# Optimization experiments

Measured on AMD Instinct MI355X. Metric: run time of the kernel, lower is better.

## Reference

```python
import jax, jax.numpy as jnp
import numpy as np


def setup_inputs() -> dict:
    key = jax.random.key(0)
    k1, k2 = jax.random.split(key)
    B, N, C, Hq, Wq = 4, 10, 256, 32, 32
    Hs, Ws = 32, 32
    return {
        "query_features": jax.random.normal(k1, (B, C, Hq, Wq), dtype=jnp.float32),
        "support_features": jax.random.normal(k2, (N, C, Hs, Ws), dtype=jnp.float32),
        "K": 5,
    }


def reference(query_features, support_features, K):
    B, C, Hq, Wq = query_features.shape
    N, _, Hs, Ws = support_features.shape
    Lq, Ls = Hq * Wq, Hs * Ws

    # [B, Lq, C] -> repeat over N -> [B*N, Lq, C]
    q = query_features.reshape(B, C, Lq).transpose(0, 2, 1)
    q = jnp.broadcast_to(q[:, None], (B, N, Lq, C)).reshape(B * N, Lq, C)
    # [N, C, Ls] -> repeat over B -> [B*N, C, Ls]
    s = support_features.reshape(N, C, Ls)
    s = jnp.broadcast_to(s[None], (B, N, C, Ls)).reshape(B * N, C, Ls)

    # global mean-centering (scalar mean over the whole repeated tensor)
    q = q - q.mean()
    s = s - s.mean()

    # unscaled similarity attention: QK^T -> softmax -> PV
    sim = jnp.einsum("bqc,bcs->bqs", q, s)          # [B*N, Lq, Ls]
    sim = jax.nn.softmax(sim, axis=-1)
    aligned = jnp.einsum("bqs,bcs->bqc", sim, s)    # [B*N, Lq, C]

    # average over K shots per class
    aligned = aligned.reshape(B, N // K, K, Hq, Wq, C).mean(axis=2)
    aligned = aligned.transpose(1, 0, 4, 2, 3)      # [N//K, B, C, Hq, Wq]

    q_out = q.transpose(0, 2, 1).reshape(B, N // K, K, C, Hq, Wq).mean(axis=2)
    # q_out: [B, N//K, C, Hq, Wq]
    return q_out, aligned
```

## Files before the change

kernel.cpp:

```cpp
#include <hip/hip_runtime.h>

#define CQ_ELEMS (4 * 256 * 1024)
#define CS_ELEMS (10 * 256 * 1024)
#define OUT2_OFF 2097152

typedef __attribute__((ext_vector_type(8))) _Float16 f16x8;
typedef __attribute__((ext_vector_type(4))) float f32x4;

#define WS_SH 256
#define SH_ELEMS (10 * 1024 * 256)
#define SV_ELEMS (10 * 256 * 1024)

__device__ __forceinline__ void gload_lds16(const unsigned short* g, unsigned short* l) {
    __builtin_amdgcn_global_load_lds(
        (const __attribute__((address_space(1))) void*)g,
        (__attribute__((address_space(3))) void*)l, 16, 0, 0);
}

__global__ __launch_bounds__(256) void means_kernel(const float* __restrict__ q,
                                                    const float* __restrict__ s,
                                                    float* __restrict__ ws) {
    const int tid = blockIdx.x * 256 + threadIdx.x;
    const int stride = gridDim.x * 256;
    float sq = 0.f, ss = 0.f;
    const float4* q4 = (const float4*)q;
    const float4* s4 = (const float4*)s;
    for (int i = tid; i < CQ_ELEMS / 4; i += stride) {
        float4 v = q4[i];
        sq += (v.x + v.y) + (v.z + v.w);
    }
    for (int i = tid; i < CS_ELEMS / 4; i += stride) {
        float4 v = s4[i];
        ss += (v.x + v.y) + (v.z + v.w);
    }
#pragma unroll
    for (int off = 32; off > 0; off >>= 1) {
        sq += __shfl_down(sq, off, 64);
        ss += __shfl_down(ss, off, 64);
    }
    __shared__ float redq[4], reds[4];
    const int lane = threadIdx.x & 63, wid = threadIdx.x >> 6;
    if (lane == 0) { redq[wid] = sq; reds[wid] = ss; }
    __syncthreads();
    if (threadIdx.x == 0) {
        atomicAdd(&ws[0], (redq[0] + redq[1]) + (redq[2] + redq[3]));
        atomicAdd(&ws[1], (reds[0] + reds[1]) + (reds[2] + reds[3]));
    }
}

__global__ __launch_bounds__(256) void convert_kernel(const float* __restrict__ Q,
                                                      const float* __restrict__ S,
                                                      const float* __restrict__ ws,
                                                      unsigned short* __restrict__ sh,
                                                      unsigned short* __restrict__ sv,
                                                      unsigned short* __restrict__ qt,
                                                      float* __restrict__ out) {
    __shared__ unsigned short Th[32][40];
    const int t = threadIdx.x;
    const int x0 = blockIdx.x << 5;
    const int c0 = blockIdx.y << 5;
    const int z = blockIdx.z;

    const int cl = t >> 3, x4 = (t & 7) << 2;

    if (z < 10) {
        const int n = z;
        const float ms = ws[1] * (1.0f / (float)CS_ELEMS);
        float4 v = *(const float4*)(S + ((size_t)(n * 256 + c0 + cl)) * 1024 + x0 + x4);
        float x[4] = {v.x - ms, v.y - ms, v.z - ms, v.w - ms};
        unsigned short hb[4];
#pragma unroll
        for (int j = 0; j < 4; ++j) {
            _Float16 h = (_Float16)x[j];
            hb[j] = __builtin_bit_cast(unsigned short, h);
            Th[cl][x4 + j] = hb[j];
        }
        *(ushort4*)(sv + ((size_t)(n * 256 + c0 + cl)) * 1024 + x0 + x4) =
            make_ushort4(hb[0], hb[1], hb[2], hb[3]);
        {
            const int lin = (z * 8 + blockIdx.y) * 32 + blockIdx.x;
            const int gid = lin * 256 + t;
            if (gid < 524288) ((int4*)(out + OUT2_OFF))[gid] = make_int4(0, 0, 0, 0);
        }
        __syncthreads();
        const int sl = t >> 3, c4 = (t & 7) << 2;
        *(ushort4*)(sh + ((size_t)(n * 1024 + x0 + sl)) * 256 + c0 + c4) =
            make_ushort4(Th[c4 + 0][sl], Th[c4 + 1][sl], Th[c4 + 2][sl], Th[c4 + 3][sl]);
    } else {
        const int b = z - 10;
        const float mq = ws[0] * (1.0f / (float)CQ_ELEMS);
        float4 v = *(const float4*)(Q + ((size_t)(b * 256 + c0 + cl)) * 1024 + x0 + x4);
        v.x -= mq; v.y -= mq; v.z -= mq; v.w -= mq;
        float* o = out + ((size_t)(b * 2) * 256 + (c0 + cl)) * 1024 + x0 + x4;
        *(float4*)o = v;
        *(float4*)(o + 256 * 1024) = v;
        float x[4] = {v.x, v.y, v.z, v.w};
#pragma unroll
        for (int j = 0; j < 4; ++j) {
            _Float16 h = (_Float16)x[j];
            Th[cl][x4 + j] = __builtin_bit_cast(unsigned short, h);
        }
        __syncthreads();
        const int ql = t >> 3, c4 = (t & 7) << 2;
        *(ushort4*)(qt + ((size_t)(b * 1024 + x0 + ql)) * 256 + c0 + c4) =
            make_ushort4(Th[c4 + 0][ql], Th[c4 + 1][ql], Th[c4 + 2][ql], Th[c4 + 3][ql]);
    }
}

union __align__(16) SMem {
    struct {
        unsigned short s1[8192];
        unsigned short s2[8192];
        unsigned short pb[64][40];
    } st;
    float epi[2][64][68];
};

__global__ __launch_bounds__(256, 3) void attn_kernel(const unsigned short* __restrict__ qt,
                                                      const unsigned short* __restrict__ sh,
                                                      const unsigned short* __restrict__ sv,
                                                      float* __restrict__ out) {
    __shared__ SMem sm;

    const int t = threadIdx.x;
    const int w = t >> 6;
    const int lane = t & 63;
    const int quad = lane >> 4;
    const int l16 = lane & 15;

    const int q0 = blockIdx.x << 6;
    const int bn = blockIdx.y;
    const int b = bn / 10;
    const int n = bn - b * 10;
    const int g = n / 5;

    const unsigned short* __restrict__ Shn = sh + (size_t)n * (1024 * 256);
    const unsigned short* __restrict__ Svn = sv + (size_t)n * (256 * 1024);

    f16x8 qf[8];
    {
        const unsigned short* qp = qt + (size_t)(b * 1024 + q0 + 16 * w + l16) * 256 + quad * 8;
#pragma unroll
        for (int f = 0; f < 8; ++f)
            qf[f] = *(const f16x8*)(qp + f * 32);
    }

    f32x4 O[4][4];
#pragma unroll
    for (int mt = 0; mt < 4; ++mt)
#pragma unroll
        for (int nt = 0; nt < 4; ++nt) O[mt][nt] = (f32x4){0.f, 0.f, 0.f, 0.f};

    float m_run[4], l_run[4];
#pragma unroll
    for (int r = 0; r < 4; ++r) { m_run[r] = -1e30f; l_run[r] = 0.f; }

    for (int s0i = 0; s0i < 32; ++s0i) {
        const int s0 = s0i << 5;
        __syncthreads();

#pragma unroll
        for (int j = 0; j < 4; ++j) {
            const int fidx = 4 * w + j;
            const unsigned short* g1 = Shn +
                (size_t)(s0 + 2 * (lane & 15) + (fidx & 1)) * 256 + (fidx >> 1) * 32 + (lane >> 4) * 8;
            gload_lds16(g1, &sm.st.s1[fidx * 512]);
            const unsigned short* g2 = Svn +
                (size_t)(w * 64 + j * 16 + (lane >> 2)) * 1024 + s0 + ((lane & 3) ^ (lane >> 4)) * 8;
            gload_lds16(g2, &sm.st.s2[fidx * 512]);
        }
        __syncthreads();

        f32x4 sim0 = (f32x4){0.f, 0.f, 0.f, 0.f};
        f32x4 sim1 = (f32x4){0.f, 0.f, 0.f, 0.f};
#pragma unroll
        for (int f = 0; f < 8; ++f) {
            const unsigned short* base = &sm.st.s1[f * 1024 + quad * 128 + l16 * 8];
            f16x8 b0 = *(const f16x8*)base;
            f16x8 b1 = *(const f16x8*)(base + 512);
            sim0 = __builtin_amdgcn_mfma_f32_16x16x32_f16(qf[f], b0, sim0, 0, 0, 0);
            sim1 = __builtin_amdgcn_mfma_f32_16x16x32_f16(qf[f], b1, sim1, 0, 0, 0);
        }

        float rowmax[4];
#pragma unroll
        for (int r = 0; r < 4; ++r) rowmax[r] = fmaxf(sim0[r], sim1[r]);
#pragma unroll
        for (int off = 1; off <= 8; off <<= 1)
#pragma unroll
            for (int r = 0; r < 4; ++r)
                rowmax[r] = fmaxf(rowmax[r], __shfl_xor(rowmax[r], off, 64));

        float al[4], rs[4], pv0[4], pv1[4];
#pragma unroll
        for (int r = 0; r < 4; ++r) {
            const float mn = fmaxf(m_run[r], rowmax[r]);
            al[r] = __expf(m_run[r] - mn);
            m_run[r] = mn;
            pv0[r] = __expf(sim0[r] - mn);
            pv1[r] = __expf(sim1[r] - mn);
            rs[r] = pv0[r] + pv1[r];
        }
#pragma unroll
        for (int off = 1; off <= 8; off <<= 1)
#pragma unroll
            for (int r = 0; r < 4; ++r) rs[r] += __shfl_xor(rs[r], off, 64);
#pragma unroll
        for (int r = 0; r < 4; ++r) l_run[r] = l_run[r] * al[r] + rs[r];

#pragma unroll
        for (int r = 0; r < 4; ++r) {
            union { _Float16 h[2]; unsigned u; } pk;
            pk.h[0] = (_Float16)pv0[r];
            pk.h[1] = (_Float16)pv1[r];
            *(unsigned*)&sm.st.pb[16 * w + 4 * quad + r][l16 * 2] = pk.u;
        }
        if (l16 == 0) {
#pragma unroll
            for (int r = 0; r < 4; ++r)
                *(float*)&sm.st.pb[16 * w + 4 * quad + r][32] = al[r];
        }
        __syncthreads();

#pragma unroll
        for (int nt = 0; nt < 4; ++nt) {
            const float a = *(const float*)&sm.st.pb[16 * nt + l16][32];
#pragma unroll
            for (int mt = 0; mt < 4; ++mt) {
                O[mt][nt][0] *= a; O[mt][nt][1] *= a; O[mt][nt][2] *= a; O[mt][nt][3] *= a;
            }
        }
        f16x8 vf[4], pf[4];
#pragma unroll
        for (int mt = 0; mt < 4; ++mt) {
            const int c = 64 * w + 16 * mt + l16;
            const int p = c * 4 + (quad ^ ((l16 >> 2) & 3));
            vf[mt] = *(const f16x8*)&sm.st.s2[p * 8];
        }
#pragma unroll
        for (int nt = 0; nt < 4; ++nt)
            pf[nt] = *(const f16x8*)&sm.st.pb[16 * nt + l16][quad * 8];
#pragma unroll
        for (int mt = 0; mt < 4; ++mt)
#pragma unroll
            for (int nt = 0; nt < 4; ++nt)
                O[mt][nt] = __builtin_amdgcn_mfma_f32_16x16x32_f16(vf[mt], pf[nt], O[mt][nt], 0, 0, 0);
    }

    if (l16 == 0) {
#pragma unroll
        for (int r = 0; r < 4; ++r)
            *(float*)&sm.st.pb[16 * w + 4 * quad + r][34] = l_run[r];
    }
    __syncthreads();

    float linv[4];
#pragma unroll
    for (int nt = 0; nt < 4; ++nt)
        linv[nt] = 0.2f / *(const float*)&sm.st.pb[16 * nt + l16][34];
    __syncthreads();

    float* __restrict__ out2 = out + OUT2_OFF + (size_t)((g << 2) + b) * (256 * 1024);

#pragma unroll
    for (int h = 0; h < 2; ++h) {
        if ((w >> 1) == h) {
            const int we = w & 1;
#pragma unroll
            for (int mt = 0; mt < 4; ++mt)
#pragma unroll
                for (int nt = 0; nt < 4; ++nt)
#pragma unroll
                    for (int r = 0; r < 4; ++r)
                        sm.epi[we][16 * mt + 4 * quad + r][16 * nt + l16] = O[mt][nt][r] * linv[nt];
        }
        __syncthreads();
#pragma unroll 4
        for (int i = 0; i < 32; ++i) {
            const int ro = w * 32 + i;
            const float v = sm.epi[ro >> 6][ro & 63][lane];
            atomicAdd(out2 + (size_t)(h * 128 + ro) * 1024 + q0 + lane, v);
        }
        __syncthreads();
    }
}

extern "C" void kernel_launch(void* const* d_in, const int* in_sizes, int n_in,
                              void* d_out, int out_size, void* d_ws, size_t ws_size,
                              hipStream_t stream) {
    const float* q = (const float*)d_in[0];
    const float* s = (const float*)d_in[1];
    float* out = (float*)d_out;
    float* ws = (float*)d_ws;
    unsigned short* sh = (unsigned short*)((char*)d_ws + WS_SH);
    unsigned short* sv = sh + SH_ELEMS;
    unsigned short* qt = sv + SV_ELEMS;

    hipMemsetAsync(d_ws, 0, 2 * sizeof(float), stream);

    means_kernel<<<256, 256, 0, stream>>>(q, s, ws);
    convert_kernel<<<dim3(32, 8, 14), 256, 0, stream>>>(q, s, ws, sh, sv, qt, out);
    attn_kernel<<<dim3(16, 40), 256, 0, stream>>>(qt, sh, sv, out);
}
```

Measured before the change: 198.2 us.

## Double-buffer K/V tiles and give each wave its own query rows in PV

Support tiles now go into two LDS buffers, so the next tile's global-to-LDS loads are issued while the current tile is computed. One barrier per iteration is removed. The PV product is reorganised so each wave owns its 16 query rows across all 256 channels, so the rescale factor and P tile no longer cross waves. The epilogue writes the whole 256x64 output block to LDS at once before the atomic adds. In exchange, LDS use roughly doubles and the occupancy hint drops from 3 to 2 blocks per CU.

```diff
diff --git a/kernel.cpp b/kernel.cpp
--- a/kernel.cpp
+++ b/kernel.cpp
@@ -109,18 +109,20 @@
 
 union __align__(16) SMem {
     struct {
-        unsigned short s1[8192];
-        unsigned short s2[8192];
+        unsigned short s1[2][8192];
+        unsigned short s2[2][8192];
         unsigned short pb[64][40];
     } st;
-    float epi[2][64][68];
+    float epi[256][68];
 };
 
-__global__ __launch_bounds__(256, 3) void attn_kernel(const unsigned short* __restrict__ qt,
+__global__ __launch_bounds__(256, 2) void attn_kernel(const unsigned short* __restrict__ qt,
                                                       const unsigned short* __restrict__ sh,
                                                       const unsigned short* __restrict__ sv,
                                                       float* __restrict__ out) {
     __shared__ SMem sm;
+    __shared__ float aw[64];
+    __shared__ float lw[64];
 
     const int t = threadIdx.x;
     const int w = t >> 6;
@@ -145,37 +147,43 @@
             qf[f] = *(const f16x8*)(qp + f * 32);
     }
 
-    f32x4 O[4][4];
-#pragma unroll
-    for (int mt = 0; mt < 4; ++mt)
-#pragma unroll
-        for (int nt = 0; nt < 4; ++nt) O[mt][nt] = (f32x4){0.f, 0.f, 0.f, 0.f};
+    f32x4 O[16];
+#pragma unroll
+    for (int mt = 0; mt < 16; ++mt) O[mt] = (f32x4){0.f, 0.f, 0.f, 0.f};
 
     float m_run[4], l_run[4];
 #pragma unroll
     for (int r = 0; r < 4; ++r) { m_run[r] = -1e30f; l_run[r] = 0.f; }
 
+#define STAGE(s0_, buf_)                                                                   \
+    {                                                                                      \
+        const int s0v = (s0_);                                                             \
+        _Pragma("unroll")                                                                  \
+        for (int j = 0; j < 4; ++j) {                                                      \
+            const int fidx = 4 * w + j;                                                    \
+            const unsigned short* g1 = Shn +                                               \
+                (size_t)(s0v + 2 * l16 + (fidx & 1)) * 256 + (fidx >> 1) * 32 + quad * 8;  \
+            gload_lds16(g1, &sm.st.s1[buf_][fidx * 512]);                                  \
+            const unsigned short* g2 = Svn +                                               \
+                (size_t)(w * 64 + j * 16 + (lane >> 2)) * 1024 + s0v +                     \
+                ((lane & 3) ^ (lane >> 4)) * 8;                                            \
+            gload_lds16(g2, &sm.st.s2[buf_][fidx * 512]);                                  \
+        }                                                                                  \
+    }
+
+    STAGE(0, 0);
+
     for (int s0i = 0; s0i < 32; ++s0i) {
-        const int s0 = s0i << 5;
+        const int cur = s0i & 1;
         __syncthreads();
 
-#pragma unroll
-        for (int j = 0; j < 4; ++j) {
-            const int fidx = 4 * w + j;
-            const unsigned short* g1 = Shn +
-                (size_t)(s0 + 2 * (lane & 15) + (fidx & 1)) * 256 + (fidx >> 1) * 32 + (lane >> 4) * 8;
-            gload_lds16(g1, &sm.st.s1[fidx * 512]);
-            const unsigned short* g2 = Svn +
-                (size_t)(w * 64 + j * 16 + (lane >> 2)) * 1024 + s0 + ((lane & 3) ^ (lane >> 4)) * 8;
-            gload_lds16(g2, &sm.st.s2[fidx * 512]);
-        }
-        __syncthreads();
+        if (s0i < 31) STAGE((s0i + 1) << 5, cur ^ 1);
 
         f32x4 sim0 = (f32x4){0.f, 0.f, 0.f, 0.f};
         f32x4 sim1 = (f32x4){0.f, 0.f, 0.f, 0.f};
 #pragma unroll
         for (int f = 0; f < 8; ++f) {
-            const unsigned short* base = &sm.st.s1[f * 1024 + quad * 128 + l16 * 8];
+            const unsigned short* base = &sm.st.s1[cur][f * 1024 + quad * 128 + l16 * 8];
             f16x8 b0 = *(const f16x8*)base;
             f16x8 b1 = *(const f16x8*)(base + 512);
             sim0 = __builtin_amdgcn_mfma_f32_16x16x32_f16(qf[f], b0, sim0, 0, 0, 0);
@@ -217,71 +225,43 @@
         }
         if (l16 == 0) {
 #pragma unroll
-            for (int r = 0; r < 4; ++r)
-                *(float*)&sm.st.pb[16 * w + 4 * quad + r][32] = al[r];
-        }
-        __syncthreads();
-
-#pragma unroll
-        for (int nt = 0; nt < 4; ++nt) {
-            const float a = *(const float*)&sm.st.pb[16 * nt + l16][32];
-#pragma unroll
-            for (int mt = 0; mt < 4; ++mt) {
-                O[mt][nt][0] *= a; O[mt][nt][1] *= a; O[mt][nt][2] *= a; O[mt][nt][3] *= a;
-            }
-        }
-        f16x8 vf[4], pf[4];
-#pragma unroll
-        for (int mt = 0; mt < 4; ++mt) {
-            const int c = 64 * w + 16 * mt + l16;
-            const int p = c * 4 + (quad ^ ((l16 >> 2) & 3));
-            vf[mt] = *(const f16x8*)&sm.st.s2[p * 8];
-        }
-#pragma unroll
-        for (int nt = 0; nt < 4; ++nt)
-            pf[nt] = *(const f16x8*)&sm.st.pb[16 * nt + l16][quad * 8];
-#pragma unroll
-        for (int mt = 0; mt < 4; ++mt)
-#pragma unroll
-            for (int nt = 0; nt < 4; ++nt)
-                O[mt][nt] = __builtin_amdgcn_mfma_f32_16x16x32_f16(vf[mt], pf[nt], O[mt][nt], 0, 0, 0);
+            for (int r = 0; r < 4; ++r) aw[16 * w + 4 * quad + r] = al[r];
+        }
+
+        const float a = aw[16 * w + l16];
+#pragma unroll
+        for (int mt = 0; mt < 16; ++mt) {
+            O[mt][0] *= a; O[mt][1] *= a; O[mt][2] *= a; O[mt][3] *= a;
+        }
+        const f16x8 pf = *(const f16x8*)&sm.st.pb[16 * w + l16][quad * 8];
+#pragma unroll
+        for (int mt = 0; mt < 16; ++mt) {
+            const int c = 16 * mt + l16;
+            const int p = c * 4 + (quad ^ (l16 >> 2));
+            f16x8 vf = *(const f16x8*)&sm.st.s2[cur][p * 8];
+            O[mt] = __builtin_amdgcn_mfma_f32_16x16x32_f16(vf, pf, O[mt], 0, 0, 0);
+        }
     }
 
     if (l16 == 0) {
 #pragma unroll
+        for (int r = 0; r < 4; ++r) lw[16 * w + 4 * quad + r] = l_run[r];
+    }
+    __syncthreads();
+    const float li = 0.2f / lw[16 * w + l16];
+
+#pragma unroll
+    for (int mt = 0; mt < 16; ++mt)
+#pragma unroll
         for (int r = 0; r < 4; ++r)
-            *(float*)&sm.st.pb[16 * w + 4 * quad + r][34] = l_run[r];
-    }
+            sm.epi[16 * mt + 4 * quad + r][16 * w + l16] = O[mt][r] * li;
     __syncthreads();
 
-    float linv[4];
-#pragma unroll
-    for (int nt = 0; nt < 4; ++nt)
-        linv[nt] = 0.2f / *(const float*)&sm.st.pb[16 * nt + l16][34];
-    __syncthreads();
-
     float* __restrict__ out2 = out + OUT2_OFF + (size_t)((g << 2) + b) * (256 * 1024);
-
-#pragma unroll
-    for (int h = 0; h < 2; ++h) {
-        if ((w >> 1) == h) {
-            const int we = w & 1;
-#pragma unroll
-            for (int mt = 0; mt < 4; ++mt)
-#pragma unroll
-                for (int nt = 0; nt < 4; ++nt)
-#pragma unroll
-                    for (int r = 0; r < 4; ++r)
-                        sm.epi[we][16 * mt + 4 * quad + r][16 * nt + l16] = O[mt][nt][r] * linv[nt];
-        }
-        __syncthreads();
 #pragma unroll 4
-        for (int i = 0; i < 32; ++i) {
-            const int ro = w * 32 + i;
-            const float v = sm.epi[ro >> 6][ro & 63][lane];
-            atomicAdd(out2 + (size_t)(h * 128 + ro) * 1024 + q0 + lane, v);
-        }
-        __syncthreads();
+    for (int i = 0; i < 64; ++i) {
+        const int c = i * 4 + w;
+        atomicAdd(out2 + (size_t)c * 1024 + q0 + lane, sm.epi[c][lane]);
     }
 }
 
```

Measured after the change: 263.0 us. 1.33x slower.

## Double-buffer key tiles in LDS and read value fragments directly from global

Applied to the files above, without the earlier changes.

The key (S1) tile is now double-buffered in LDS, and the next tile's global-to-LDS load is issued before the current tile's QK^T MFMAs so the transfer overlaps compute. The value tile no longer goes through LDS: each lane loads its f16x8 fragment straight from global memory right before the PV MFMAs. The per-iteration barrier after staging is gone, and the row-scale and row-sum values move to small dedicated shared arrays, which also removes one epilogue barrier. In exchange, global-load latency for V now sits on the critical path with a strided access pattern. Correctness also depends on the async LDS loads completing before the next iteration's barrier.

```diff
diff --git a/kernel.cpp b/kernel.cpp
--- a/kernel.cpp
+++ b/kernel.cpp
@@ -109,8 +109,7 @@
 
 union __align__(16) SMem {
     struct {
-        unsigned short s1[8192];
-        unsigned short s2[8192];
+        unsigned short s1[2][8192];
         unsigned short pb[64][40];
     } st;
     float epi[2][64][68];
@@ -121,6 +120,8 @@
                                                       const unsigned short* __restrict__ sv,
                                                       float* __restrict__ out) {
     __shared__ SMem sm;
+    __shared__ float aw[64];
+    __shared__ float lw[64];
 
     const int t = threadIdx.x;
     const int w = t >> 6;
@@ -145,6 +146,11 @@
             qf[f] = *(const f16x8*)(qp + f * 32);
     }
 
+    const unsigned short* vbase[4];
+#pragma unroll
+    for (int mt = 0; mt < 4; ++mt)
+        vbase[mt] = Svn + (size_t)(64 * w + 16 * mt + l16) * 1024 + quad * 8;
+
     f32x4 O[4][4];
 #pragma unroll
     for (int mt = 0; mt < 4; ++mt)
@@ -155,27 +161,32 @@
 #pragma unroll
     for (int r = 0; r < 4; ++r) { m_run[r] = -1e30f; l_run[r] = 0.f; }
 
+#define STAGE1(s0_, buf_)                                                                  \
+    {                                                                                      \
+        const int s0v = (s0_);                                                             \
+        _Pragma("unroll")                                                                  \
+        for (int j = 0; j < 4; ++j) {                                                      \
+            const int fidx = 4 * w + j;                                                    \
+            const unsigned short* g1 = Shn +                                               \
+                (size_t)(s0v + 2 * l16 + (fidx & 1)) * 256 + (fidx >> 1) * 32 + quad * 8;  \
+            gload_lds16(g1, &sm.st.s1[buf_][fidx * 512]);                                  \
+        }                                                                                  \
+    }
+
+    STAGE1(0, 0);
+
     for (int s0i = 0; s0i < 32; ++s0i) {
+        const int cur = s0i & 1;
         const int s0 = s0i << 5;
         __syncthreads();
 
-#pragma unroll
-        for (int j = 0; j < 4; ++j) {
-            const int fidx = 4 * w + j;
-            const unsigned short* g1 = Shn +
-                (size_t)(s0 + 2 * (lane & 15) + (fidx & 1)) * 256 + (fidx >> 1) * 32 + (lane >> 4) * 8;
-            gload_lds16(g1, &sm.st.s1[fidx * 512]);
-            const unsigned short* g2 = Svn +
-                (size_t)(w * 64 + j * 16 + (lane >> 2)) * 1024 + s0 + ((lane & 3) ^ (lane >> 4)) * 8;
-            gload_lds16(g2, &sm.st.s2[fidx * 512]);
-        }
-        __syncthreads();
+        if (s0i < 31) STAGE1((s0i + 1) << 5, cur ^ 1);
 
         f32x4 sim0 = (f32x4){0.f, 0.f, 0.f, 0.f};
         f32x4 sim1 = (f32x4){0.f, 0.f, 0.f, 0.f};
 #pragma unroll
         for (int f = 0; f < 8; ++f) {
-            const unsigned short* base = &sm.st.s1[f * 1024 + quad * 128 + l16 * 8];
+            const unsigned short* base = &sm.st.s1[cur][f * 1024 + quad * 128 + l16 * 8];
             f16x8 b0 = *(const f16x8*)base;
             f16x8 b1 = *(const f16x8*)(base + 512);
             sim0 = __builtin_amdgcn_mfma_f32_16x16x32_f16(qf[f], b0, sim0, 0, 0, 0);
@@ -217,48 +228,40 @@
         }
         if (l16 == 0) {
 #pragma unroll
-            for (int r = 0; r < 4; ++r)
-                *(float*)&sm.st.pb[16 * w + 4 * quad + r][32] = al[r];
+            for (int r = 0; r < 4; ++r) aw[16 * w + 4 * quad + r] = al[r];
         }
         __syncthreads();
 
 #pragma unroll
         for (int nt = 0; nt < 4; ++nt) {
-            const float a = *(const float*)&sm.st.pb[16 * nt + l16][32];
+            const float a = aw[16 * nt + l16];
 #pragma unroll
             for (int mt = 0; mt < 4; ++mt) {
                 O[mt][nt][0] *= a; O[mt][nt][1] *= a; O[mt][nt][2] *= a; O[mt][nt][3] *= a;
             }
         }
-        f16x8 vf[4], pf[4];
-#pragma unroll
-        for (int mt = 0; mt < 4; ++mt) {
-            const int c = 64 * w + 16 * mt + l16;
-            const int p = c * 4 + (quad ^ ((l16 >> 2) & 3));
-            vf[mt] = *(const f16x8*)&sm.st.s2[p * 8];
-        }
+        f16x8 pf[4];
 #pragma unroll
         for (int nt = 0; nt < 4; ++nt)
             pf[nt] = *(const f16x8*)&sm.st.pb[16 * nt + l16][quad * 8];
 #pragma unroll
-        for (int mt = 0; mt < 4; ++mt)
+        for (int mt = 0; mt < 4; ++mt) {
+            f16x8 vf = *(const f16x8*)(vbase[mt] + s0);
 #pragma unroll
             for (int nt = 0; nt < 4; ++nt)
-                O[mt][nt] = __builtin_amdgcn_mfma_f32_16x16x32_f16(vf[mt], pf[nt], O[mt][nt], 0, 0, 0);
+                O[mt][nt] = __builtin_amdgcn_mfma_f32_16x16x32_f16(vf, pf[nt], O[mt][nt], 0, 0, 0);
+        }
     }
 
     if (l16 == 0) {
 #pragma unroll
-        for (int r = 0; r < 4; ++r)
-            *(float*)&sm.st.pb[16 * w + 4 * quad + r][34] = l_run[r];
+        for (int r = 0; r < 4; ++r) lw[16 * w + 4 * quad + r] = l_run[r];
     }
     __syncthreads();
 
     float linv[4];
 #pragma unroll
-    for (int nt = 0; nt < 4; ++nt)
-        linv[nt] = 0.2f / *(const float*)&sm.st.pb[16 * nt + l16][34];
-    __syncthreads();
+    for (int nt = 0; nt < 4; ++nt) linv[nt] = 0.2f / lw[16 * nt + l16];
 
     float* __restrict__ out2 = out + OUT2_OFF + (size_t)((g << 2) + b) * (256 * 1024);
 
```

Result: slower. 211.7 us (+6.8%).
